# Optimization experiments

Hardware: AMD Instinct MI355X
Metric: run time of the kernel (lower is better)

Reference implementation:

```python
import jax, jax.numpy as jnp
import numpy as np

N_FEATS = 256
N_HEAD = 8
EPS_LN = 1e-5  # nn.LayerNorm default eps (both per-head K/V norms and final LN)


def sine_pos_embed(h, w, num_pos_feats, dtype=jnp.float32):
    """DETR PositionEmbeddingSine with normalize=True, mask=None -> [h, w, 2*num_pos_feats]."""
    eps = 1e-6
    scale = 2.0 * np.pi
    temperature = 10000.0
    # cumsum of ones == arange(1, n+1); normalized by last value (= h or w) + eps
    y = (jnp.arange(1, h + 1, dtype=dtype) / (h + eps) * scale)[:, None, None]  # [h,1,1]
    x = (jnp.arange(1, w + 1, dtype=dtype) / (w + eps) * scale)[None, :, None]  # [1,w,1]
    dim_t = jnp.arange(num_pos_feats, dtype=dtype)
    dim_t = temperature ** (2.0 * jnp.floor(dim_t / 2.0) / num_pos_feats)

    def interleave(t):
        # stack(sin(t[0::2]), cos(t[1::2])).flatten -> sin,cos interleaved
        return jnp.stack((jnp.sin(t[..., 0::2]), jnp.cos(t[..., 1::2])), axis=-1).reshape(
            t.shape[:-1] + (num_pos_feats,))

    py = jnp.broadcast_to(interleave(y / dim_t), (h, w, num_pos_feats))
    px = jnp.broadcast_to(interleave(x / dim_t), (h, w, num_pos_feats))
    return jnp.concatenate((py, px), axis=-1)  # channel order: [pos_y, pos_x]


def _ln(t, g, b, eps=EPS_LN):
    mu = jnp.mean(t, axis=-1, keepdims=True)
    var = jnp.var(t, axis=-1, keepdims=True)
    return (t - mu) * jax.lax.rsqrt(var + eps) * g + b


def setup_inputs() -> dict:
    key = jax.random.key(0)
    ks = jax.random.split(key, 4)
    b, c, h, w = 8, N_FEATS, 128, 128
    d_k = c // N_HEAD
    s = 0.02
    return dict(
        x=jax.random.normal(ks[0], (b, c, h, w), jnp.float32),
        Wq=jax.random.normal(ks[1], (c, c), jnp.float32) * s,
        bq=jnp.zeros((c,), jnp.float32),
        Wk=jax.random.normal(ks[2], (c, c), jnp.float32) * s,
        bk=jnp.zeros((c,), jnp.float32),
        Wv=jax.random.normal(ks[3], (c, c), jnp.float32) * s,
        bv=jnp.zeros((c,), jnp.float32),
        gK=jnp.ones((N_HEAD, d_k), jnp.float32),
        bK=jnp.zeros((N_HEAD, d_k), jnp.float32),
        gV=jnp.ones((N_HEAD, d_k), jnp.float32),
        bV=jnp.zeros((N_HEAD, d_k), jnp.float32),
        g_ln=jnp.ones((c,), jnp.float32),
        b_ln=jnp.zeros((c,), jnp.float32),
    )


def reference(x, Wq, bq, Wk, bk, Wv, bv, gK, bK, gV, bV, g_ln, b_ln):
    b, c, h, w = x.shape
    d_k = c // N_HEAD
    n = h * w
    pos = sine_pos_embed(h, w, c // 2, dtype=x.dtype).reshape(1, n, c)
    xs = jnp.transpose(x, (0, 2, 3, 1)).reshape(b, n, c)  # [b, n, c]
    qk_in = xs + pos

    def proj(t, W, bias):
        # torch Linear: t @ W.T + b, then split heads -> [b, H, n, d_k]
        return (t @ W.T + bias).reshape(b, n, N_HEAD, d_k).transpose(0, 2, 1, 3)

    q = proj(qk_in, Wq, bq)
    k = proj(qk_in, Wk, bk)
    v = proj(xs, Wv, bv)

    # galerkin: per-head LayerNorm over d_k on K and V (learnable per-head affine)
    k = _ln(k, gK[None, :, None, :], bK[None, :, None, :])
    v = _ln(v, gV[None, :, None, :], bV[None, :, None, :])

    # linear (galerkin) attention: Q @ (K^T V) / seq_len  (attn dropout p=0.0)
    scores = jnp.einsum('bhnd,bhne->bhde', k, v) / n  # [b, H, d_k, d_k]
    out = jnp.einsum('bhnd,bhde->bhne', q, scores)    # [b, H, n, d_k]
    out = out.transpose(0, 2, 1, 3).reshape(b, n, c)

    out = out + out  # x = x + dropout(x); dropout identity at inference
    out = _ln(out, g_ln, b_ln)
    return jnp.transpose(out.reshape(b, h, w, c), (0, 3, 1, 2))  # [b, c, h, w]
```

## Files before the change

### kernel.cpp

```cpp
#include <hip/hip_runtime.h>


typedef float floatx4 __attribute__((ext_vector_type(4)));
typedef __bf16 bf16x8 __attribute__((ext_vector_type(8)));
typedef unsigned short ushortx8 __attribute__((ext_vector_type(8)));
typedef unsigned short ushort;

static __device__ __forceinline__ ushort f2bf(float f) {
  unsigned int u = __builtin_bit_cast(unsigned int, f);
  u += 0x7FFFu + ((u >> 16) & 1u);
  return (ushort)(u >> 16);
}
static __device__ __forceinline__ float bf2f(ushort u) {
  unsigned int x = ((unsigned int)u) << 16;
  return __builtin_bit_cast(float, x);
}
static __device__ __forceinline__ floatx4 mfma16(bf16x8 a, bf16x8 b, floatx4 c) {
  return __builtin_amdgcn_mfma_f32_16x16x32_bf16(a, b, c, 0, 0, 0);
}
static __device__ __forceinline__ bf16x8 frag(const ushort* p) {
  return *(const bf16x8*)p;
}
typedef __attribute__((address_space(3))) unsigned int as3_u32;
typedef __attribute__((address_space(1))) const unsigned int as1_u32;
static __device__ __forceinline__ void gl_lds16(const ushort* g, ushort* l) {
  __builtin_amdgcn_global_load_lds((as1_u32*)g, (as3_u32*)l, 16, 0, 0);
}

__global__ __launch_bounds__(256) void prep_w(const float* __restrict__ Wk,
                                              const float* __restrict__ Wv,
                                              ushort* __restrict__ Wkbf,
                                              ushort* __restrict__ Wvbf) {
  const int i = (int)blockIdx.x * 256 + (int)threadIdx.x;
  float4 a = ((const float4*)Wk)[i];
  float4 b = ((const float4*)Wv)[i];
  ushort4 ua = {f2bf(a.x), f2bf(a.y), f2bf(a.z), f2bf(a.w)};
  ushort4 ub = {f2bf(b.x), f2bf(b.y), f2bf(b.z), f2bf(b.w)};
  ((ushort4*)Wkbf)[i] = ua;
  ((ushort4*)Wvbf)[i] = ub;
}

__global__ __launch_bounds__(256) void poswk(const float* __restrict__ Wk,
                                             const float* __restrict__ bk,
                                             float* __restrict__ PyKb,
                                             float* __restrict__ PxKj) {
  __shared__ float pe[128];
  const int ii = (int)blockIdx.x, t = (int)threadIdx.x;
  if (t < 128) {
    const float coord = (float)(ii + 1) * (6.283185307179586f / (128.0f + 1e-6f));
    const float inv = exp2f(-13.287712379549449f * (float)(t >> 1) * (1.0f / 64.0f));
    const float arg = coord * inv;
    pe[t] = (t & 1) ? cosf(arg) : sinf(arg);
  }
  __syncthreads();
  const float* wrow = Wk + (size_t)t * 256;
  float py = bk[t], px = 0.0f;
#pragma unroll 8
  for (int kk = 0; kk < 128; ++kk) {
    py += pe[kk] * wrow[kk];
    px += pe[kk] * wrow[128 + kk];
  }
  PyKb[ii * 256 + t] = py;
  PxKj[ii * 256 + t] = px;
}

__global__ __launch_bounds__(256) void posw2(const ushort* __restrict__ W2bf,
                                             const float* __restrict__ b2,
                                             float* __restrict__ Py2b,
                                             float* __restrict__ Px2T) {
  __shared__ float pe[128];
  const int ii = (int)blockIdx.x, z = (int)blockIdx.y, t = (int)threadIdx.x;
  if (t < 128) {
    const float coord = (float)(ii + 1) * (6.283185307179586f / (128.0f + 1e-6f));
    const float inv = exp2f(-13.287712379549449f * (float)(t >> 1) * (1.0f / 64.0f));
    const float arg = coord * inv;
    pe[t] = (t & 1) ? cosf(arg) : sinf(arg);
  }
  __syncthreads();
  const ushort* wrow = W2bf + (size_t)z * 65536 + (size_t)t * 256;
  float py = b2[z * 256 + t], px = 0.0f;
#pragma unroll 8
  for (int kk = 0; kk < 128; ++kk) {
    py += pe[kk] * bf2f(wrow[kk]);
    px += pe[kk] * bf2f(wrow[128 + kk]);
  }
  Py2b[((size_t)z * 128 + ii) * 256 + t] = py;
  Px2T[(size_t)z * 32768 + t * 128 + ii] = px;
}

__global__ __launch_bounds__(256) void prep_qx(const float* __restrict__ x,
                                               ushort* __restrict__ xT, int b0) {
  __shared__ float tile[64 * 68];
  const int t = (int)threadIdx.x;
  const int z = (int)blockIdx.y;
  const int b = b0 + z;
  const int n0 = (int)blockIdx.x * 64;
  const float* xb = x + (size_t)b * 256 * 16384;
  ushort* xtb = xT + (size_t)z * 16384 * 256;
  for (int kc = 0; kc < 4; ++kc) {
    if (kc) __syncthreads();
    const int nn = (t & 15) * 4;
    const int r0 = t >> 4;
#pragma unroll
    for (int it = 0; it < 4; ++it) {
      const int k = r0 + it * 16;
      const float4 v = *(const float4*)(xb + (size_t)(kc * 64 + k) * 16384 + n0 + nn);
      tile[(nn + 0) * 68 + k] = v.x;
      tile[(nn + 1) * 68 + k] = v.y;
      tile[(nn + 2) * 68 + k] = v.z;
      tile[(nn + 3) * 68 + k] = v.w;
    }
    __syncthreads();
#pragma unroll
    for (int it = 0; it < 2; ++it) {
      const int P = t + it * 256;
      const int r = P >> 3;
      const int p = P & 7;
      const int n = n0 + r;
      ushortx8 ux;
#pragma unroll
      for (int e = 0; e < 8; ++e) ux[e] = f2bf(tile[r * 68 + p * 8 + e]);
      const int sw = (p ^ (r & 7)) * 8;
      *(ushortx8*)(xtb + (size_t)n * 256 + kc * 64 + sw) = ux;
    }
  }
}

#define LDC2 40
#define NT 4
__global__ __launch_bounds__(512, 2) void kv_scores(
    const ushort* __restrict__ xT, const ushort* __restrict__ Wkbf,
    const ushort* __restrict__ Wvbf, const float* __restrict__ bv,
    const float* __restrict__ gK, const float* __restrict__ bKp,
    const float* __restrict__ gV, const float* __restrict__ bVp,
    const float* __restrict__ PyKb, const float* __restrict__ PxKj,
    float* __restrict__ partials) {
  __shared__ ushort SQ[2][128 * 64];
  __shared__ ushort KT[256 * LDC2];
  __shared__ ushort VT[256 * LDC2];
  const int t = (int)threadIdx.x, lane = t & 63, w = t >> 6;
  const int l15 = lane & 15, l4 = lane >> 4;
  const int z = (int)blockIdx.y;
  const int bx = (int)blockIdx.x;
  const ushort* xb = xT + (size_t)z * 16384 * 256;
  const int ocb = w * 32;
  const int h = w;
  const int oc4 = ocb + l4 * 4;
  const floatx4 bv4[2] = {*(const floatx4*)(bv + oc4),
                          *(const floatx4*)(bv + oc4 + 16)};
  const int hb = h * 32 + l4 * 4;
  const floatx4 gk4[2] = {*(const floatx4*)(gK + hb), *(const floatx4*)(gK + hb + 16)};
  const floatx4 ok4[2] = {*(const floatx4*)(bKp + hb), *(const floatx4*)(bKp + hb + 16)};
  const floatx4 gv4[2] = {*(const floatx4*)(gV + hb), *(const floatx4*)(gV + hb + 16)};
  const floatx4 ov4[2] = {*(const floatx4*)(bVp + hb), *(const floatx4*)(bVp + hb + 16)};
  const int srow = w * 16 + (lane >> 3);
  const int scol = (lane & 7) * 8;
  const int rsw = l15 & 7;

  auto issue = [&](int s) {
    const int n0s = (bx * NT + (s >> 2)) * 128;
    const int kcs = (s & 3) * 64;
    ushort* dst = &SQ[s & 1][w * 1024];
    const ushort* src = xb + (size_t)(n0s + srow) * 256 + kcs + scol;
#pragma unroll
    for (int j = 0; j < 2; ++j) gl_lds16(src + (size_t)j * 8 * 256, dst + j * 512);
  };
  issue(0);

  floatx4 sacc[2][2] = {};
  for (int nt = 0; nt < NT; ++nt) {
    const int i_nt = bx * NT + nt;
    floatx4 acck[2][8] = {};
    floatx4 accv[2][8] = {};
    for (int kc = 0; kc < 4; ++kc) {
      const int s = nt * 4 + kc;
      __syncthreads();
      bf16x8 Ak0[2], Ak1[2], Av0[2], Av1[2];
#pragma unroll
      for (int ci = 0; ci < 2; ++ci) {
        const int kb = (kc * 2 + ci) * 32 + l4 * 8;
        Ak0[ci] = frag(Wkbf + (ocb + l15) * 256 + kb);
        Ak1[ci] = frag(Wkbf + (ocb + 16 + l15) * 256 + kb);
        Av0[ci] = frag(Wvbf + (ocb + l15) * 256 + kb);
        Av1[ci] = frag(Wvbf + (ocb + 16 + l15) * 256 + kb);
      }
      if (s < NT * 4 - 1) issue(s + 1);
      const ushort* sq = &SQ[s & 1][0];
      __builtin_amdgcn_s_setprio(1);
#pragma unroll
      for (int ci = 0; ci < 2; ++ci) {
#pragma unroll
        for (int m = 0; m < 8; ++m) {
          const int off = (m * 16 + l15) * 64 + ((ci * 4 + l4) ^ rsw) * 8;
          const bf16x8 b = *(const bf16x8*)(sq + off);
          acck[0][m] = mfma16(Ak0[ci], b, acck[0][m]);
          acck[1][m] = mfma16(Ak1[ci], b, acck[1][m]);
          accv[0][m] = mfma16(Av0[ci], b, accv[0][m]);
          accv[1][m] = mfma16(Av1[ci], b, accv[1][m]);
        }
      }
      __builtin_amdgcn_s_setprio(0);
    }
    const floatx4 pyk[2] = {*(const floatx4*)(PyKb + i_nt * 256 + oc4),
                            *(const floatx4*)(PyKb + i_nt * 256 + oc4 + 16)};
#pragma unroll
    for (int q = 0; q < 4; ++q) {
#pragma unroll
      for (int mm = 0; mm < 2; ++mm) {
        const int m = q * 2 + mm;
        const floatx4 pxk0 = *(const floatx4*)(PxKj + (m * 16 + l15) * 256 + oc4);
        const floatx4 pxk1 = *(const floatx4*)(PxKj + (m * 16 + l15) * 256 + oc4 + 16);
        float s0 = 0.0f, q0 = 0.0f;
#pragma unroll
        for (int r = 0; r < 4; ++r) {
          acck[0][m][r] += pyk[0][r] + pxk0[r];
          acck[1][m][r] += pyk[1][r] + pxk1[r];
          const float v0 = acck[0][m][r], v1 = acck[1][m][r];
          s0 += v0 + v1;
          q0 += v0 * v0 + v1 * v1;
        }
        s0 += __shfl_xor(s0, 16); s0 += __shfl_xor(s0, 32);
        q0 += __shfl_xor(q0, 16); q0 += __shfl_xor(q0, 32);
        {
          const float mu = s0 * (1.0f / 32.0f);
          const float rstd = rsqrtf(q0 * (1.0f / 32.0f) - mu * mu + 1e-5f);
#pragma unroll
          for (int tt = 0; tt < 2; ++tt)
#pragma unroll
            for (int r = 0; r < 4; ++r)
              acck[tt][m][r] = (acck[tt][m][r] - mu) * rstd * gk4[tt][r] + ok4[tt][r];
        }
        float s1 = 0.0f, q1 = 0.0f;
#pragma unroll
        for (int r = 0; r < 4; ++r) {
          accv[0][m][r] += bv4[0][r];
          accv[1][m][r] += bv4[1][r];
          const float v0 = accv[0][m][r], v1 = accv[1][m][r];
          s1 += v0 + v1;
          q1 += v0 * v0 + v1 * v1;
        }
        s1 += __shfl_xor(s1, 16); s1 += __shfl_xor(s1, 32);
        q1 += __shfl_xor(q1, 16); q1 += __shfl_xor(q1, 32);
        {
          const float mu = s1 * (1.0f / 32.0f);
          const float rstd = rsqrtf(q1 * (1.0f / 32.0f) - mu * mu + 1e-5f);
#pragma unroll
          for (int tt = 0; tt < 2; ++tt)
#pragma unroll
            for (int r = 0; r < 4; ++r)
              accv[tt][m][r] = (accv[tt][m][r] - mu) * rstd * gv4[tt][r] + ov4[tt][r];
        }
#pragma unroll
        for (int tt = 0; tt < 2; ++tt) {
          const int ch = w * 32 + tt * 16 + l4 * 4;
#pragma unroll
          for (int r = 0; r < 4; ++r) {
            KT[(ch + r) * LDC2 + mm * 16 + l15] = f2bf(acck[tt][m][r]);
            VT[(ch + r) * LDC2 + mm * 16 + l15] = f2bf(accv[tt][m][r]);
          }
        }
      }
      const int ko = l4 * 8;
      const bf16x8 ka0 = *(const bf16x8*)(KT + (w * 32 + l15) * LDC2 + ko);
      const bf16x8 ka1 = *(const bf16x8*)(KT + (w * 32 + 16 + l15) * LDC2 + ko);
      const bf16x8 vb0 = *(const bf16x8*)(VT + (w * 32 + l15) * LDC2 + ko);
      const bf16x8 vb1 = *(const bf16x8*)(VT + (w * 32 + 16 + l15) * LDC2 + ko);
      sacc[0][0] = mfma16(ka0, vb0, sacc[0][0]);
      sacc[0][1] = mfma16(ka0, vb1, sacc[0][1]);
      sacc[1][0] = mfma16(ka1, vb0, sacc[1][0]);
      sacc[1][1] = mfma16(ka1, vb1, sacc[1][1]);
    }
  }
  float* pp = partials + (((size_t)z * 8 + h) * 32 + bx) * 1024;
#pragma unroll
  for (int di = 0; di < 2; ++di)
#pragma unroll
    for (int ej = 0; ej < 2; ++ej)
#pragma unroll
      for (int r = 0; r < 4; ++r)
        pp[(di * 16 + l4 * 4 + r) * 32 + ej * 16 + l15] = sacc[di][ej][r];
}

__global__ __launch_bounds__(256) void reduce_scores(
    const float* __restrict__ partials, float* __restrict__ scores) {
  const int h = (int)blockIdx.x, z = (int)blockIdx.y, t = (int)threadIdx.x;
  const float* pb = partials + ((size_t)(z * 8 + h) * 32) * 1024 + t * 4;
  float4 s = {0.0f, 0.0f, 0.0f, 0.0f};
#pragma unroll 8
  for (int bx = 0; bx < 32; ++bx) {
    const float4 v = *(const float4*)(pb + bx * 1024);
    s.x += v.x; s.y += v.y; s.z += v.z; s.w += v.w;
  }
  *(float4*)(scores + (size_t)(z * 8 + h) * 1024 + t * 4) = s;
}

__global__ __launch_bounds__(256) void w2_kernel(
    const float* __restrict__ Wq, const float* __restrict__ bq,
    const float* __restrict__ scores, ushort* __restrict__ W2bf,
    float* __restrict__ b2) {
  const int z = (int)blockIdx.y;
  const int row = (int)blockIdx.x;
  const int t = (int)threadIdx.x;
  const float inv_n = 1.0f / 16384.0f;
  const float* sc = scores + (size_t)z * 8192;
  if (row < 256) {
    const int h = row >> 5, e = row & 31;
    float s = 0.0f;
#pragma unroll
    for (int d = 0; d < 32; ++d)
      s += Wq[(h * 32 + d) * 256 + t] * sc[(h * 32 + d) * 32 + e];
    W2bf[(size_t)z * 65536 + row * 256 + t] = f2bf(s * inv_n);
  } else {
    const int h = t >> 5, e = t & 31;
    float s = 0.0f;
#pragma unroll
    for (int d = 0; d < 32; ++d)
      s += bq[h * 32 + d] * sc[(h * 32 + d) * 32 + e];
    b2[z * 256 + t] = s * inv_n;
  }
}

__global__ __launch_bounds__(256, 2) void out_kernel(
    const ushort* __restrict__ xT, const ushort* __restrict__ W2bf,
    const float* __restrict__ Py2b, const float* __restrict__ Px2T,
    const float* __restrict__ g_ln, const float* __restrict__ b_ln,
    float* __restrict__ out, int b0) {
  const int t = (int)threadIdx.x, lane = t & 63, w = t >> 6;
  const int l15 = lane & 15, l4 = lane >> 4;
  const int z = (int)blockIdx.y, b = b0 + z;
  const int bx = (int)blockIdx.x;
  const int n0 = bx * 64;
  const ushort* xb = xT + (size_t)z * 16384 * 256;
  const ushort* W2b = W2bf + (size_t)z * 65536;
  const float* py = Py2b + ((size_t)z * 128 + (bx >> 1)) * 256;
  const float* pxT = Px2T + (size_t)z * 32768;
  const int jbase = (bx & 1) * 64 + w * 16 + l4 * 4;
  const int row = n0 + w * 16 + l15;
  const int rsw = l15 & 7;
  floatx4 acc[16] = {};
#pragma unroll
  for (int c = 0; c < 8; ++c) {
    const int kb = c * 32 + l4 * 8;
    const int off = (c >> 1) * 64 + ((((c & 1) * 4 + l4) ^ rsw)) * 8;
    const bf16x8 a = frag(xb + (size_t)row * 256 + off);
#pragma unroll
    for (int tt = 0; tt < 16; ++tt) {
      const bf16x8 bb = frag(W2b + (tt * 16 + l15) * 256 + kb);
      acc[tt] = mfma16(a, bb, acc[tt]);
    }
  }
#pragma unroll
  for (int tt = 0; tt < 16; ++tt) {
    const int c = tt * 16 + l15;
    const float pyv = py[c];
    const float4 px = *(const float4*)(pxT + c * 128 + jbase);
    const float pxa[4] = {px.x, px.y, px.z, px.w};
#pragma unroll
    for (int r = 0; r < 4; ++r) acc[tt][r] = 2.0f * (acc[tt][r] + pyv + pxa[r]);
  }
  float mean[4], rstd[4];
#pragma unroll
  for (int r = 0; r < 4; ++r) {
    float s = 0.0f, q = 0.0f;
#pragma unroll
    for (int tt = 0; tt < 16; ++tt) {
      const float v = acc[tt][r];
      s += v;
      q += v * v;
    }
#pragma unroll
    for (int msk = 1; msk < 16; msk <<= 1) {
      s += __shfl_xor(s, msk);
      q += __shfl_xor(q, msk);
    }
    const float mu = s * (1.0f / 256.0f);
    mean[r] = mu;
    rstd[r] = rsqrtf(q * (1.0f / 256.0f) - mu * mu + 1e-5f);
  }
#pragma unroll
  for (int tt = 0; tt < 16; ++tt) {
    const int c = tt * 16 + l15;
    const float g = g_ln[c], be = b_ln[c];
    float4 o;
    o.x = (acc[tt][0] - mean[0]) * rstd[0] * g + be;
    o.y = (acc[tt][1] - mean[1]) * rstd[1] * g + be;
    o.z = (acc[tt][2] - mean[2]) * rstd[2] * g + be;
    o.w = (acc[tt][3] - mean[3]) * rstd[3] * g + be;
    *(float4*)(out + (size_t)(b * 256 + c) * 16384 + n0 + w * 16 + l4 * 4) = o;
  }
}

extern "C" void kernel_launch(void* const* d_in, const int* in_sizes, int n_in,
                              void* d_out, int out_size, void* d_ws, size_t ws_size,
                              hipStream_t stream) {
  (void)in_sizes; (void)n_in; (void)out_size;
  const float* x   = (const float*)d_in[0];
  const float* Wq  = (const float*)d_in[1];
  const float* bq  = (const float*)d_in[2];
  const float* Wk  = (const float*)d_in[3];
  const float* bk  = (const float*)d_in[4];
  const float* Wv  = (const float*)d_in[5];
  const float* bv  = (const float*)d_in[6];
  const float* gK  = (const float*)d_in[7];
  const float* bK  = (const float*)d_in[8];
  const float* gV  = (const float*)d_in[9];
  const float* bV  = (const float*)d_in[10];
  const float* gln = (const float*)d_in[11];
  const float* bln = (const float*)d_in[12];
  float* out = (float*)d_out;

  const size_t PB = 16384ULL * 256 * 2;
  const size_t PERZ = PB + 131072 + 131072 + 131072 + 1048576 + 32768 + 1024;
  const size_t SHARED = 262144 + 262144;
  int g = 8;
  while (g > 1 && ws_size < (size_t)g * PERZ + SHARED) g >>= 1;

  char* p = (char*)d_ws;
  ushort* xT    = (ushort*)p; p += (size_t)g * PB;
  ushort* Wkbf  = (ushort*)p; p += 131072;
  ushort* Wvbf  = (ushort*)p; p += 131072;
  float*  PyKb  = (float*)p;  p += 131072;
  float*  PxKj  = (float*)p;  p += 131072;
  ushort* W2bf  = (ushort*)p; p += (size_t)g * 131072;
  float*  Py2b  = (float*)p;  p += (size_t)g * 131072;
  float*  Px2T  = (float*)p;  p += (size_t)g * 131072;
  float*  partials = (float*)p; p += (size_t)g * 1048576;
  float*  scores = (float*)p; p += (size_t)g * 32768;
  float*  b2    = (float*)p;

  prep_w<<<dim3(64), 256, 0, stream>>>(Wk, Wv, Wkbf, Wvbf);
  poswk<<<dim3(128), 256, 0, stream>>>(Wk, bk, PyKb, PxKj);
  for (int b0 = 0; b0 < 8; b0 += g) {
    prep_qx<<<dim3(256, g), 256, 0, stream>>>(x, xT, b0);
    kv_scores<<<dim3(32, g), 512, 0, stream>>>(xT, Wkbf, Wvbf, bv, gK, bK,
                                               gV, bV, PyKb, PxKj, partials);
    reduce_scores<<<dim3(8, g), 256, 0, stream>>>(partials, scores);
    w2_kernel<<<dim3(257, g), 256, 0, stream>>>(Wq, bq, scores, W2bf, b2);
    posw2<<<dim3(128, g), 256, 0, stream>>>(W2bf, b2, Py2b, Px2T);
    out_kernel<<<dim3(256, g), 256, 0, stream>>>(xT, W2bf, Py2b, Px2T, gln, bln,
                                                 out, b0);
  }
}
```

Measured before the change: 586.9 us.

## Restructure output GEMM with LDS double-buffered xT tiles and cross-wave LayerNorm

Rewrites out_kernel so 512-thread blocks process four 128-row tiles, streaming xT chunks into double-buffered LDS via async global-to-LDS loads while W2 fragments stay in registers per wave. LayerNorm statistics are reduced across waves through shared memory, and the Px positional term is stored row-major to match the new access pattern. The aim is better reuse of W2 and overlapped loads; the risks are a small grid of 32 blocks per batch and narrower scalar output stores.

New measurement: 503.2 us. 1.17x faster.

```diff
diff --git a/kernel.cpp b/kernel.cpp
--- a/kernel.cpp
+++ b/kernel.cpp
@@ -67,7 +67,7 @@
 __global__ __launch_bounds__(256) void posw2(const ushort* __restrict__ W2bf,
                                              const float* __restrict__ b2,
                                              float* __restrict__ Py2b,
-                                             float* __restrict__ Px2T) {
+                                             float* __restrict__ Px2j) {
   __shared__ float pe[128];
   const int ii = (int)blockIdx.x, z = (int)blockIdx.y, t = (int)threadIdx.x;
   if (t < 128) {
@@ -85,7 +85,7 @@
     px += pe[kk] * bf2f(wrow[128 + kk]);
   }
   Py2b[((size_t)z * 128 + ii) * 256 + t] = py;
-  Px2T[(size_t)z * 32768 + t * 128 + ii] = px;
+  Px2j[((size_t)z * 128 + ii) * 256 + t] = px;
 }
 
 __global__ __launch_bounds__(256) void prep_qx(const float* __restrict__ x,
@@ -320,73 +320,115 @@
   }
 }
 
-__global__ __launch_bounds__(256, 2) void out_kernel(
+#define ONT 4
+__global__ __launch_bounds__(512, 2) void out_kernel(
     const ushort* __restrict__ xT, const ushort* __restrict__ W2bf,
-    const float* __restrict__ Py2b, const float* __restrict__ Px2T,
+    const float* __restrict__ Py2b, const float* __restrict__ Px2j,
     const float* __restrict__ g_ln, const float* __restrict__ b_ln,
     float* __restrict__ out, int b0) {
+  __shared__ ushort SQ[2][128 * 64];
+  __shared__ float redS[8][136];
+  __shared__ float redQ[8][136];
   const int t = (int)threadIdx.x, lane = t & 63, w = t >> 6;
   const int l15 = lane & 15, l4 = lane >> 4;
   const int z = (int)blockIdx.y, b = b0 + z;
   const int bx = (int)blockIdx.x;
-  const int n0 = bx * 64;
   const ushort* xb = xT + (size_t)z * 16384 * 256;
   const ushort* W2b = W2bf + (size_t)z * 65536;
-  const float* py = Py2b + ((size_t)z * 128 + (bx >> 1)) * 256;
-  const float* pxT = Px2T + (size_t)z * 32768;
-  const int jbase = (bx & 1) * 64 + w * 16 + l4 * 4;
-  const int row = n0 + w * 16 + l15;
+  const int ocb = w * 32;
+  const int oc4 = ocb + l4 * 4;
+  const floatx4 gl4[2] = {*(const floatx4*)(g_ln + oc4),
+                          *(const floatx4*)(g_ln + oc4 + 16)};
+  const floatx4 bl4[2] = {*(const floatx4*)(b_ln + oc4),
+                          *(const floatx4*)(b_ln + oc4 + 16)};
+  const int srow = w * 16 + (lane >> 3);
+  const int scol = (lane & 7) * 8;
   const int rsw = l15 & 7;
-  floatx4 acc[16] = {};
-#pragma unroll
-  for (int c = 0; c < 8; ++c) {
-    const int kb = c * 32 + l4 * 8;
-    const int off = (c >> 1) * 64 + ((((c & 1) * 4 + l4) ^ rsw)) * 8;
-    const bf16x8 a = frag(xb + (size_t)row * 256 + off);
-#pragma unroll
-    for (int tt = 0; tt < 16; ++tt) {
-      const bf16x8 bb = frag(W2b + (tt * 16 + l15) * 256 + kb);
-      acc[tt] = mfma16(a, bb, acc[tt]);
-    }
-  }
-#pragma unroll
-  for (int tt = 0; tt < 16; ++tt) {
-    const int c = tt * 16 + l15;
-    const float pyv = py[c];
-    const float4 px = *(const float4*)(pxT + c * 128 + jbase);
-    const float pxa[4] = {px.x, px.y, px.z, px.w};
-#pragma unroll
-    for (int r = 0; r < 4; ++r) acc[tt][r] = 2.0f * (acc[tt][r] + pyv + pxa[r]);
-  }
-  float mean[4], rstd[4];
-#pragma unroll
-  for (int r = 0; r < 4; ++r) {
-    float s = 0.0f, q = 0.0f;
-#pragma unroll
-    for (int tt = 0; tt < 16; ++tt) {
-      const float v = acc[tt][r];
-      s += v;
-      q += v * v;
-    }
-#pragma unroll
-    for (int msk = 1; msk < 16; msk <<= 1) {
-      s += __shfl_xor(s, msk);
-      q += __shfl_xor(q, msk);
-    }
-    const float mu = s * (1.0f / 256.0f);
-    mean[r] = mu;
-    rstd[r] = rsqrtf(q * (1.0f / 256.0f) - mu * mu + 1e-5f);
-  }
-#pragma unroll
-  for (int tt = 0; tt < 16; ++tt) {
-    const int c = tt * 16 + l15;
-    const float g = g_ln[c], be = b_ln[c];
-    float4 o;
-    o.x = (acc[tt][0] - mean[0]) * rstd[0] * g + be;
-    o.y = (acc[tt][1] - mean[1]) * rstd[1] * g + be;
-    o.z = (acc[tt][2] - mean[2]) * rstd[2] * g + be;
-    o.w = (acc[tt][3] - mean[3]) * rstd[3] * g + be;
-    *(float4*)(out + (size_t)(b * 256 + c) * 16384 + n0 + w * 16 + l4 * 4) = o;
+
+  auto issue = [&](int s) {
+    const int n0s = (bx * ONT + (s >> 2)) * 128;
+    const int kcs = (s & 3) * 64;
+    ushort* dst = &SQ[s & 1][w * 1024];
+    const ushort* src = xb + (size_t)(n0s + srow) * 256 + kcs + scol;
+#pragma unroll
+    for (int j = 0; j < 2; ++j) gl_lds16(src + (size_t)j * 8 * 256, dst + j * 512);
+  };
+  issue(0);
+
+  for (int nt = 0; nt < ONT; ++nt) {
+    const int i_nt = bx * ONT + nt;
+    const int n0 = i_nt * 128;
+    floatx4 acc[2][8] = {};
+    for (int kc = 0; kc < 4; ++kc) {
+      const int s = nt * 4 + kc;
+      __syncthreads();
+      bf16x8 A0[2], A1[2];
+#pragma unroll
+      for (int ci = 0; ci < 2; ++ci) {
+        const int kb = (kc * 2 + ci) * 32 + l4 * 8;
+        A0[ci] = frag(W2b + (ocb + l15) * 256 + kb);
+        A1[ci] = frag(W2b + (ocb + 16 + l15) * 256 + kb);
+      }
+      if (s < ONT * 4 - 1) issue(s + 1);
+      const ushort* sq = &SQ[s & 1][0];
+      __builtin_amdgcn_s_setprio(1);
+#pragma unroll
+      for (int ci = 0; ci < 2; ++ci) {
+#pragma unroll
+        for (int m = 0; m < 8; ++m) {
+          const int off = (m * 16 + l15) * 64 + ((ci * 4 + l4) ^ rsw) * 8;
+          const bf16x8 bb = *(const bf16x8*)(sq + off);
+          acc[0][m] = mfma16(A0[ci], bb, acc[0][m]);
+          acc[1][m] = mfma16(A1[ci], bb, acc[1][m]);
+        }
+      }
+      __builtin_amdgcn_s_setprio(0);
+    }
+    const floatx4 py[2] = {
+        *(const floatx4*)(Py2b + ((size_t)z * 128 + i_nt) * 256 + oc4),
+        *(const floatx4*)(Py2b + ((size_t)z * 128 + i_nt) * 256 + oc4 + 16)};
+#pragma unroll
+    for (int m = 0; m < 8; ++m) {
+      const float* pxr = Px2j + ((size_t)z * 128 + m * 16 + l15) * 256;
+      const floatx4 px0 = *(const floatx4*)(pxr + oc4);
+      const floatx4 px1 = *(const floatx4*)(pxr + oc4 + 16);
+      float s = 0.0f, q = 0.0f;
+#pragma unroll
+      for (int r = 0; r < 4; ++r) {
+        const float v0 = 2.0f * (acc[0][m][r] + py[0][r] + px0[r]);
+        const float v1 = 2.0f * (acc[1][m][r] + py[1][r] + px1[r]);
+        acc[0][m][r] = v0;
+        acc[1][m][r] = v1;
+        s += v0 + v1;
+        q += v0 * v0 + v1 * v1;
+      }
+      s += __shfl_xor(s, 16); s += __shfl_xor(s, 32);
+      q += __shfl_xor(q, 16); q += __shfl_xor(q, 32);
+      if (l4 == 0) {
+        redS[w][m * 16 + l15] = s;
+        redQ[w][m * 16 + l15] = q;
+      }
+    }
+    __syncthreads();
+#pragma unroll
+    for (int m = 0; m < 8; ++m) {
+      const int nr = m * 16 + l15;
+      float S = 0.0f, Q = 0.0f;
+#pragma unroll
+      for (int ww = 0; ww < 8; ++ww) {
+        S += redS[ww][nr];
+        Q += redQ[ww][nr];
+      }
+      const float mu = S * (1.0f / 256.0f);
+      const float rstd = rsqrtf(Q * (1.0f / 256.0f) - mu * mu + 1e-5f);
+#pragma unroll
+      for (int tt = 0; tt < 2; ++tt)
+#pragma unroll
+        for (int r = 0; r < 4; ++r) {
+          const float o = (acc[tt][m][r] - mu) * rstd * gl4[tt][r] + bl4[tt][r];
+          out[(size_t)(b * 256 + oc4 + tt * 16 + r) * 16384 + n0 + nr] = o;
+        }
+    }
   }
 }
 
@@ -423,7 +465,7 @@
   float*  PxKj  = (float*)p;  p += 131072;
   ushort* W2bf  = (ushort*)p; p += (size_t)g * 131072;
   float*  Py2b  = (float*)p;  p += (size_t)g * 131072;
-  float*  Px2T  = (float*)p;  p += (size_t)g * 131072;
+  float*  Px2j  = (float*)p;  p += (size_t)g * 131072;
   float*  partials = (float*)p; p += (size_t)g * 1048576;
   float*  scores = (float*)p; p += (size_t)g * 32768;
   float*  b2    = (float*)p;
@@ -436,8 +478,8 @@
                                                gV, bV, PyKb, PxKj, partials);
     reduce_scores<<<dim3(8, g), 256, 0, stream>>>(partials, scores);
     w2_kernel<<<dim3(257, g), 256, 0, stream>>>(Wq, bq, scores, W2bf, b2);
-    posw2<<<dim3(128, g), 256, 0, stream>>>(W2bf, b2, Py2b, Px2T);
-    out_kernel<<<dim3(256, g), 256, 0, stream>>>(xT, W2bf, Py2b, Px2T, gln, bln,
-                                                 out, b0);
-  }
-}
+    posw2<<<dim3(128, g), 256, 0, stream>>>(W2bf, b2, Py2b, Px2j);
+    out_kernel<<<dim3(32, g), 512, 0, stream>>>(xT, W2bf, Py2b, Px2j, gln, bln,
+                                                out, b0);
+  }
+}
```
